# Kernel optimization log

Hardware: AMD Instinct MI355X
Metric: run time of the kernel (lower is better)

Reference implementation:

```python
import jax, jax.numpy as jnp
import numpy as np

B, S, D, F, E, K = 4, 2048, 1024, 2048, 8, 2


def setup_inputs() -> dict:
    key = jax.random.key(0)
    ks = jax.random.split(key, 6)
    s_in = 1.0 / np.sqrt(D)
    s_ff = 1.0 / np.sqrt(F)
    return {
        "x": jax.random.normal(ks[0], (B, S, D), jnp.float32),
        "rms_w": jnp.ones((D,), jnp.float32),
        "Wg": jax.random.normal(ks[1], (D, E), jnp.float32) * s_in,
        "bg": jnp.zeros((E,), jnp.float32),
        "W1a": jax.random.normal(ks[2], (E, D, F), jnp.float32) * s_in,
        "b1a": jnp.zeros((E, F), jnp.float32),
        "W1b": jax.random.normal(ks[3], (E, D, F), jnp.float32) * s_in,
        "b1b": jnp.zeros((E, F), jnp.float32),
        "W2": jax.random.normal(ks[4], (E, F, D), jnp.float32) * s_ff,
        "b2": jnp.zeros((E, D), jnp.float32),
    }


def reference(x, rms_w, Wg, bg, W1a, b1a, W1b, b1b, W2, b2):
    # RMSNorm (torch nn.RMSNorm with eps=None -> finfo eps)
    eps = jnp.finfo(x.dtype).eps
    x = x * jax.lax.rsqrt(jnp.mean(x * x, axis=-1, keepdims=True) + eps) * rms_w

    # top-k gating
    logits = x @ Wg + bg                              # [B,S,E]
    topk_vals, topk_idx = jax.lax.top_k(logits, K)    # [B,S,K]
    topk_w = jax.nn.softmax(topk_vals, axis=-1)       # [B,S,K]
    one_hot = jax.nn.one_hot(topk_idx, E, dtype=x.dtype)  # [B,S,K,E]
    weights = jnp.sum(one_hot * topk_w[..., None], axis=2)  # [B,S,E]

    # dense per-expert SwiGLU (faithful to the masked dense loop)
    a = jnp.einsum("bsd,edf->bsef", x, W1a) + b1a     # [B,S,E,F]
    b = jnp.einsum("bsd,edf->bsef", x, W1b) + b1b
    h = jax.nn.silu(a) * b
    y = jnp.einsum("bsef,efd->bsed", h, W2) + b2      # [B,S,E,D]
    out = jnp.einsum("bse,bsed->bsd", weights, y)     # [B,S,D]
    return out, weights
```

## Files before the change

### kernel.cpp

```cpp
#include <hip/hip_runtime.h>
#include <hip/hip_bf16.h>

#define DD 1024
#define FF 2048
#define EE 8
#define NT 8192
#define NRCAP 17280
#define MAXT128 135

typedef __attribute__((ext_vector_type(8))) short bf16x8;
typedef __attribute__((ext_vector_type(4))) float f32x4;

__device__ __forceinline__ ushort f2bf(float f) {
  __hip_bfloat16 h = __float2bfloat16(f);
  return *reinterpret_cast<ushort*>(&h);
}

__device__ __forceinline__ void gload16(const void* g, void* l) {
  __builtin_amdgcn_global_load_lds((const __attribute__((address_space(1))) void*)g,
                                   (__attribute__((address_space(3))) void*)l, 16, 0, 0);
}

__device__ __forceinline__ int swz_of_row(int r) { return ((r >> 1) & 3) << 4; }

__global__ __launch_bounds__(256) void k_transpose_all(
    const float* __restrict__ W1a, const float* __restrict__ W1b,
    const float* __restrict__ W2, ushort* __restrict__ BT1, ushort* __restrict__ W2T) {
  __shared__ ushort tile[64][68];
  const int z = blockIdx.z;
  const int cq = threadIdx.x & 15, rr = threadIdx.x >> 4;
  if (z < 16) {
    const int half = z >> 3, e = z & 7;
    const float* ip = (half ? W1b : W1a) + (size_t)e * DD * FF;
    const int f0 = blockIdx.x * 64, d0 = blockIdx.y * 64;
    #pragma unroll
    for (int p = 0; p < 4; p++) {
      const int r = rr + 16 * p;
      float4 v = *reinterpret_cast<const float4*>(ip + (size_t)(d0 + r) * FF + f0 + 4 * cq);
      *reinterpret_cast<ushort4*>(&tile[r][4 * cq]) =
          make_ushort4(f2bf(v.x), f2bf(v.y), f2bf(v.z), f2bf(v.w));
    }
    __syncthreads();
    ushort* op = BT1 + (size_t)e * 4096 * DD;
    const int rq = threadIdx.x & 15, cc = threadIdx.x >> 4;
    #pragma unroll
    for (int p = 0; p < 4; p++) {
      const int f = f0 + cc + 16 * p;
      const int rmap = ((f >> 4) << 5) + half * 16 + (f & 15);
      ushort4 u = make_ushort4(tile[4 * rq + 0][cc + 16 * p], tile[4 * rq + 1][cc + 16 * p],
                               tile[4 * rq + 2][cc + 16 * p], tile[4 * rq + 3][cc + 16 * p]);
      *reinterpret_cast<ushort4*>(op + (size_t)rmap * DD + d0 + 4 * rq) = u;
    }
  } else {
    const int e = z & 7;
    const float* ip = W2 + (size_t)e * FF * DD;
    const int r0 = blockIdx.x * 64;
    const int c0 = blockIdx.y * 64;
    #pragma unroll
    for (int p = 0; p < 4; p++) {
      const int r = rr + 16 * p;
      float4 v = *reinterpret_cast<const float4*>(ip + (size_t)(r0 + r) * DD + c0 + 4 * cq);
      *reinterpret_cast<ushort4*>(&tile[r][4 * cq]) =
          make_ushort4(f2bf(v.x), f2bf(v.y), f2bf(v.z), f2bf(v.w));
    }
    __syncthreads();
    ushort* op = W2T + (size_t)e * DD * FF;
    const int rq = threadIdx.x & 15, cc = threadIdx.x >> 4;
    #pragma unroll
    for (int p = 0; p < 4; p++) {
      const int c = cc + 16 * p;
      ushort4 u = make_ushort4(tile[4 * rq + 0][c], tile[4 * rq + 1][c],
                               tile[4 * rq + 2][c], tile[4 * rq + 3][c]);
      *reinterpret_cast<ushort4*>(op + (size_t)(c0 + c) * FF + r0 + 4 * rq) = u;
    }
  }
}

__global__ __launch_bounds__(256) void k_rms_gate(
    const float* __restrict__ x, const float* __restrict__ rms_w,
    const float* __restrict__ Wg, const float* __restrict__ bg,
    ushort* __restrict__ xn, float* __restrict__ out0, float* __restrict__ outW,
    int* __restrict__ tk_e, float* __restrict__ tk_w) {
  const int t = blockIdx.x * 4 + (threadIdx.x >> 6);
  const int lane = threadIdx.x & 63;
  const float* xrow = x + (size_t)t * DD;
  const float4* x4 = reinterpret_cast<const float4*>(xrow);
  const float4* w4 = reinterpret_cast<const float4*>(rms_w);
  const float4* Wg4 = reinterpret_cast<const float4*>(Wg);
  float4 xv[4];
  float ss = 0.f;
  #pragma unroll
  for (int i = 0; i < 4; i++) {
    xv[i] = x4[i * 64 + lane];
    ss += xv[i].x * xv[i].x + xv[i].y * xv[i].y + xv[i].z * xv[i].z + xv[i].w * xv[i].w;
  }
  #pragma unroll
  for (int m = 32; m; m >>= 1) ss += __shfl_xor(ss, m);
  const float sc = 1.0f / sqrtf(ss * (1.0f / (float)DD) + 1.1920929e-07f);
  ushort4* xout = reinterpret_cast<ushort4*>(xn + (size_t)t * DD);
  float4* orow = reinterpret_cast<float4*>(out0 + (size_t)t * DD);
  #pragma unroll
  for (int i = 0; i < 4; i++) {
    const float4 wv = w4[i * 64 + lane];
    xout[i * 64 + lane] = make_ushort4(f2bf(xv[i].x * sc * wv.x), f2bf(xv[i].y * sc * wv.y),
                                       f2bf(xv[i].z * sc * wv.z), f2bf(xv[i].w * sc * wv.w));
    orow[i * 64 + lane] = make_float4(0.f, 0.f, 0.f, 0.f);
  }
  float4 lgv = make_float4(0.f, 0.f, 0.f, 0.f);
  #pragma unroll 8
  for (int k = 0; k < 32; k++) {
    const int d = (lane >> 1) + 32 * k;
    const float s = xrow[d] * sc * rms_w[d];
    const float4 wg = Wg4[lane + 64 * k];
    lgv.x += s * wg.x; lgv.y += s * wg.y; lgv.z += s * wg.z; lgv.w += s * wg.w;
  }
  #pragma unroll
  for (int m = 32; m >= 2; m >>= 1) {
    lgv.x += __shfl_xor(lgv.x, m);
    lgv.y += __shfl_xor(lgv.y, m);
    lgv.z += __shfl_xor(lgv.z, m);
    lgv.w += __shfl_xor(lgv.w, m);
  }
  float4 other;
  other.x = __shfl(lgv.x, lane ^ 1);
  other.y = __shfl(lgv.y, lane ^ 1);
  other.z = __shfl(lgv.z, lane ^ 1);
  other.w = __shfl(lgv.w, lane ^ 1);
  if (lane == 0) {
    float l[8] = { lgv.x + bg[0], lgv.y + bg[1], lgv.z + bg[2], lgv.w + bg[3],
                   other.x + bg[4], other.y + bg[5], other.z + bg[6], other.w + bg[7] };
    int i0 = 0; float v0 = l[0];
    #pragma unroll
    for (int i = 1; i < 8; i++) if (l[i] > v0) { v0 = l[i]; i0 = i; }
    int i1 = -1; float v1 = -3.4e38f;
    #pragma unroll
    for (int i = 0; i < 8; i++) if (i != i0 && l[i] > v1) { v1 = l[i]; i1 = i; }
    const float e1v = __expf(v1 - v0);
    const float w0 = 1.0f / (1.0f + e1v);
    const float w1 = e1v * w0;
    float wout[8] = {0.f, 0.f, 0.f, 0.f, 0.f, 0.f, 0.f, 0.f};
    wout[i0] = w0; wout[i1] = w1;
    float4* wrow = reinterpret_cast<float4*>(outW + (size_t)t * EE);
    wrow[0] = make_float4(wout[0], wout[1], wout[2], wout[3]);
    wrow[1] = make_float4(wout[4], wout[5], wout[6], wout[7]);
    tk_e[t] = i0 | (i1 << 8);
    tk_w[2 * t] = w0; tk_w[2 * t + 1] = w1;
  }
}

__global__ __launch_bounds__(256) void k_scatter(
    const int* __restrict__ tk_e, const float* __restrict__ tk_w, int* __restrict__ base,
    int* __restrict__ tok_of_row, float* __restrict__ gw_of_row) {
  const int e = blockIdx.x;
  const int tid = threadIdx.x, wid = tid >> 6, lane = tid & 63;
  int c[8] = {0, 0, 0, 0, 0, 0, 0, 0};
  for (int i = tid; i < NT; i += 256) {
    const int ee = tk_e[i];
    c[ee & 255]++;
    c[(ee >> 8) & 255]++;
  }
  #pragma unroll
  for (int m = 32; m; m >>= 1) {
    #pragma unroll
    for (int i = 0; i < 8; i++) c[i] += __shfl_xor(c[i], m);
  }
  __shared__ int sw[4][8];
  __shared__ int s_base[9];
  if (lane == 0) {
    #pragma unroll
    for (int i = 0; i < 8; i++) sw[wid][i] = c[i];
  }
  __syncthreads();
  if (tid == 0) {
    int acc = 0;
    for (int q = 0; q < EE; q++) {
      s_base[q] = acc;
      const int cnt = sw[0][q] + sw[1][q] + sw[2][q] + sw[3][q];
      acc += ((cnt + 127) >> 7) << 7;
    }
    s_base[EE] = acc;
  }
  __syncthreads();
  if (e == 0 && tid <= EE) base[tid] = s_base[tid];
  const int myBase = s_base[e], myEnd = s_base[e + 1];
  for (int i = myBase + tid; i < myEnd; i += 256) tok_of_row[i] = -1;
  __syncthreads();
  __shared__ int s_cursor;
  __shared__ int s_woff[4];
  if (tid == 0) s_cursor = myBase;
  __syncthreads();
  for (int t0 = 0; t0 < NT; t0 += 256) {
    const int t = t0 + tid;
    const int ee = tk_e[t];
    const int m0 = (ee & 255) == e;
    const int m1 = ((ee >> 8) & 255) == e;
    const int has = m0 | m1;
    const unsigned long long mask = __ballot(has);
    const int prefix = __popcll(mask & ((1ull << lane) - 1ull));
    if (lane == 0) s_woff[wid] = __popcll(mask);
    __syncthreads();
    int woff = 0;
    #pragma unroll
    for (int w = 0; w < 4; w++) woff += (w < wid) ? s_woff[w] : 0;
    if (has) {
      const int row = s_cursor + woff + prefix;
      tok_of_row[row] = t;
      gw_of_row[row] = tk_w[2 * t + (m0 ? 0 : 1)];
    }
    __syncthreads();
    if (tid == 0) s_cursor += s_woff[0] + s_woff[1] + s_woff[2] + s_woff[3];
  }
}

__global__ __launch_bounds__(256) void k_ffn1(
    const ushort* __restrict__ xn, const ushort* __restrict__ BT1,
    const float* __restrict__ b1a, const float* __restrict__ b1b,
    const int* __restrict__ tok_of_row, const int* __restrict__ base,
    ushort* __restrict__ H) {
  const int row0 = blockIdx.y * 128;
  if (row0 >= base[EE]) return;
  int e = 0;
  while (e < EE - 1 && row0 >= base[e + 1]) e++;
  const int c0 = blockIdx.x * 128;
  const int tid = threadIdx.x, wid = tid >> 6, lane = tid & 63;
  const int wr = wid >> 1, wc = wid & 1;
  __shared__ __align__(16) ushort smem[128 * 72];
  ushort* sA = smem;
  ushort* sB = smem + 4096;
  const int rloc = tid >> 2;
  const int kcol = (((tid & 3) * 16) ^ swz_of_row(rloc)) >> 1;
  int tok0 = tok_of_row[row0 + rloc];      if (tok0 < 0) tok0 = 0;
  int tok1 = tok_of_row[row0 + 64 + rloc]; if (tok1 < 0) tok1 = 0;
  const ushort* gA0 = xn + (size_t)tok0 * DD + kcol;
  const ushort* gA1 = xn + (size_t)tok1 * DD + kcol;
  const ushort* gB0 = BT1 + ((size_t)e * 4096 + c0 + rloc) * DD + kcol;
  const ushort* gB1 = BT1 + ((size_t)e * 4096 + c0 + 64 + rloc) * DD + kcol;
  ushort* lA0 = sA + wid * 512;  ushort* lA1 = sA + 2048 + wid * 512;
  ushort* lB0 = sB + wid * 512;  ushort* lB1 = sB + 2048 + wid * 512;
  const int lrow = lane & 15, q = lane >> 4;
  const int fsw = (q * 16) ^ swz_of_row(lrow);
  int aoff[4], boff[4];
  #pragma unroll
  for (int m = 0; m < 4; m++) aoff[m] = (wr * 64 + m * 16 + lrow) * 64 + fsw;
  #pragma unroll
  for (int n = 0; n < 4; n++) boff[n] = (wc * 64 + n * 16 + lrow) * 64 + fsw;
  f32x4 acc[16];
  #pragma unroll
  for (int i = 0; i < 16; i++) acc[i] = (f32x4){0.f, 0.f, 0.f, 0.f};
  for (int kt = 0; kt < DD / 32; kt++) {
    gload16(gA0 + kt * 32, lA0);
    gload16(gA1 + kt * 32, lA1);
    gload16(gB0 + kt * 32, lB0);
    gload16(gB1 + kt * 32, lB1);
    __syncthreads();
    bf16x8 fb[4];
    #pragma unroll
    for (int n = 0; n < 4; n++)
      fb[n] = *reinterpret_cast<const bf16x8*>(reinterpret_cast<const char*>(sB) + boff[n]);
    #pragma unroll
    for (int m = 0; m < 4; m++) {
      const bf16x8 fa = *reinterpret_cast<const bf16x8*>(reinterpret_cast<const char*>(sA) + aoff[m]);
      #pragma unroll
      for (int n = 0; n < 4; n++)
        acc[m * 4 + n] = __builtin_amdgcn_mfma_f32_16x16x32_bf16(fa, fb[n], acc[m * 4 + n], 0, 0, 0);
    }
    __syncthreads();
  }
  #pragma unroll
  for (int np = 0; np < 2; np++) {
    const int fl = wc * 32 + np * 16 + lrow;
    const int f = (c0 >> 1) + fl;
    const float ba_ = b1a[e * FF + f], bb_ = b1b[e * FF + f];
    #pragma unroll
    for (int m = 0; m < 4; m++) {
      #pragma unroll
      for (int r = 0; r < 4; r++) {
        const float a = acc[m * 4 + 2 * np][r] + ba_;
        const float b = acc[m * 4 + 2 * np + 1][r] + bb_;
        const float h = (a / (1.0f + __expf(-a))) * b;
        const int rl = wr * 64 + m * 16 + q * 4 + r;
        smem[rl * 72 + fl] = f2bf(h);
      }
    }
  }
  __syncthreads();
  const int fc = tid & 7, rb = tid >> 3;
  #pragma unroll
  for (int i = 0; i < 4; i++) {
    const int rl = i * 32 + rb;
    const uint4 v = *reinterpret_cast<const uint4*>(&smem[rl * 72 + fc * 8]);
    *reinterpret_cast<uint4*>(H + (size_t)(row0 + rl) * FF + (c0 >> 1) + fc * 8) = v;
  }
}

__global__ __launch_bounds__(256) void k_ffn2(
    const ushort* __restrict__ H, const ushort* __restrict__ W2T, const float* __restrict__ b2,
    const int* __restrict__ tok_of_row, const float* __restrict__ gw_of_row,
    const int* __restrict__ base, float* __restrict__ out0) {
  const int row0 = blockIdx.y * 128;
  if (row0 >= base[EE]) return;
  int e = 0;
  while (e < EE - 1 && row0 >= base[e + 1]) e++;
  const int d0 = blockIdx.x * 128;
  const int tid = threadIdx.x, wid = tid >> 6, lane = tid & 63;
  const int wr = wid >> 1, wc = wid & 1;
  __shared__ ushort sA[128 * 32], sB[128 * 32];
  const int rloc = tid >> 2;
  const int kcol = (((tid & 3) * 16) ^ swz_of_row(rloc)) >> 1;
  const ushort* gA0 = H + (size_t)(row0 + rloc) * FF + kcol;
  const ushort* gA1 = H + (size_t)(row0 + 64 + rloc) * FF + kcol;
  const ushort* gB0 = W2T + ((size_t)e * DD + d0 + rloc) * FF + kcol;
  const ushort* gB1 = W2T + ((size_t)e * DD + d0 + 64 + rloc) * FF + kcol;
  ushort* lA0 = sA + wid * 512;  ushort* lA1 = sA + 2048 + wid * 512;
  ushort* lB0 = sB + wid * 512;  ushort* lB1 = sB + 2048 + wid * 512;
  const int lrow = lane & 15, q = lane >> 4;
  const int fsw = (q * 16) ^ swz_of_row(lrow);
  int aoff[4], boff[4];
  #pragma unroll
  for (int m = 0; m < 4; m++) aoff[m] = (wr * 64 + m * 16 + lrow) * 64 + fsw;
  #pragma unroll
  for (int n = 0; n < 4; n++) boff[n] = (wc * 64 + n * 16 + lrow) * 64 + fsw;
  f32x4 acc[16];
  #pragma unroll
  for (int i = 0; i < 16; i++) acc[i] = (f32x4){0.f, 0.f, 0.f, 0.f};
  for (int kt = 0; kt < FF / 32; kt++) {
    gload16(gA0 + kt * 32, lA0);
    gload16(gA1 + kt * 32, lA1);
    gload16(gB0 + kt * 32, lB0);
    gload16(gB1 + kt * 32, lB1);
    __syncthreads();
    bf16x8 fb[4];
    #pragma unroll
    for (int n = 0; n < 4; n++)
      fb[n] = *reinterpret_cast<const bf16x8*>(reinterpret_cast<const char*>(sB) + boff[n]);
    #pragma unroll
    for (int m = 0; m < 4; m++) {
      const bf16x8 fa = *reinterpret_cast<const bf16x8*>(reinterpret_cast<const char*>(sA) + aoff[m]);
      #pragma unroll
      for (int n = 0; n < 4; n++)
        acc[m * 4 + n] = __builtin_amdgcn_mfma_f32_16x16x32_bf16(fa, fb[n], acc[m * 4 + n], 0, 0, 0);
    }
    __syncthreads();
  }
  int dcols[4]; float bias[4];
  #pragma unroll
  for (int n = 0; n < 4; n++) {
    dcols[n] = d0 + wc * 64 + n * 16 + lrow;
    bias[n] = b2[e * DD + dcols[n]];
  }
  #pragma unroll
  for (int m = 0; m < 4; m++) {
    #pragma unroll
    for (int r = 0; r < 4; r++) {
      const int grow = row0 + wr * 64 + m * 16 + q * 4 + r;
      const int tk = tok_of_row[grow];
      if (tk >= 0) {
        const float gw = gw_of_row[grow];
        float* orow = out0 + (size_t)tk * DD;
        #pragma unroll
        for (int n = 0; n < 4; n++)
          atomicAdd(orow + dcols[n], gw * (acc[m * 4 + n][r] + bias[n]));
      }
    }
  }
}

#define WS_XN   ((size_t)0)
#define WS_BT1  ((size_t)16777216)
#define WS_W2T  ((size_t)83886080)
#define WS_H    ((size_t)117440512)
#define WS_TOK  ((size_t)188219392)
#define WS_GW   ((size_t)188288512)
#define WS_TKE  ((size_t)188357632)
#define WS_TKW  ((size_t)188390400)
#define WS_BASE ((size_t)188455936)

extern "C" void kernel_launch(void* const* d_in, const int* in_sizes, int n_in,
                              void* d_out, int out_size, void* d_ws, size_t ws_size,
                              hipStream_t stream) {
  const float* x     = (const float*)d_in[0];
  const float* rms_w = (const float*)d_in[1];
  const float* Wg    = (const float*)d_in[2];
  const float* bg    = (const float*)d_in[3];
  const float* W1a   = (const float*)d_in[4];
  const float* b1a   = (const float*)d_in[5];
  const float* W1b   = (const float*)d_in[6];
  const float* b1b   = (const float*)d_in[7];
  const float* W2    = (const float*)d_in[8];
  const float* b2    = (const float*)d_in[9];
  float* out0 = (float*)d_out;
  float* outW = (float*)d_out + (size_t)NT * DD;

  char* ws = (char*)d_ws;
  ushort* xn    = (ushort*)(ws + WS_XN);
  ushort* BT1   = (ushort*)(ws + WS_BT1);
  ushort* W2T   = (ushort*)(ws + WS_W2T);
  ushort* Hbuf  = (ushort*)(ws + WS_H);
  int*    tok   = (int*)(ws + WS_TOK);
  float*  gw    = (float*)(ws + WS_GW);
  int*    tk_e  = (int*)(ws + WS_TKE);
  float*  tk_w  = (float*)(ws + WS_TKW);
  int*    base  = (int*)(ws + WS_BASE);

  k_transpose_all<<<dim3(32, 16, 24), 256, 0, stream>>>(W1a, W1b, W2, BT1, W2T);

  k_rms_gate<<<NT / 4, 256, 0, stream>>>(x, rms_w, Wg, bg, xn, out0, outW, tk_e, tk_w);
  k_scatter<<<EE, 256, 0, stream>>>(tk_e, tk_w, base, tok, gw);

  k_ffn1<<<dim3(4096 / 128, MAXT128), 256, 0, stream>>>(xn, BT1, b1a, b1b, tok, base, Hbuf);
  k_ffn2<<<dim3(DD / 128, MAXT128), 256, 0, stream>>>(Hbuf, W2T, b2, tok, gw, base, out0);
}
```

Before: 436.0 us.

## Replace atomic scatter-add in FFN2 with dense Y buffer plus per-token gather

FFN2 now writes its per-row expert outputs plus bias into a dense fp32 Y buffer instead of doing gate-weighted atomicAdds into the output. A new gather kernel then combines each token's two rows with its top-k weights. The scatter kernel records the Y row for each token slot instead of a per-row gate weight, and the output zero-init in rms_gate is dropped. This removes atomic contention and the zeroing pass. In exchange it costs a roughly 70MB intermediate write and read, one extra launch, and a Y buffer that aliases the xn/BT1 workspace.

```diff
diff --git a/kernel.cpp b/kernel.cpp
--- a/kernel.cpp
+++ b/kernel.cpp
@@ -79,7 +79,7 @@
 __global__ __launch_bounds__(256) void k_rms_gate(
     const float* __restrict__ x, const float* __restrict__ rms_w,
     const float* __restrict__ Wg, const float* __restrict__ bg,
-    ushort* __restrict__ xn, float* __restrict__ out0, float* __restrict__ outW,
+    ushort* __restrict__ xn, float* __restrict__ outW,
     int* __restrict__ tk_e, float* __restrict__ tk_w) {
   const int t = blockIdx.x * 4 + (threadIdx.x >> 6);
   const int lane = threadIdx.x & 63;
@@ -98,13 +98,11 @@
   for (int m = 32; m; m >>= 1) ss += __shfl_xor(ss, m);
   const float sc = 1.0f / sqrtf(ss * (1.0f / (float)DD) + 1.1920929e-07f);
   ushort4* xout = reinterpret_cast<ushort4*>(xn + (size_t)t * DD);
-  float4* orow = reinterpret_cast<float4*>(out0 + (size_t)t * DD);
   #pragma unroll
   for (int i = 0; i < 4; i++) {
     const float4 wv = w4[i * 64 + lane];
     xout[i * 64 + lane] = make_ushort4(f2bf(xv[i].x * sc * wv.x), f2bf(xv[i].y * sc * wv.y),
                                        f2bf(xv[i].z * sc * wv.z), f2bf(xv[i].w * sc * wv.w));
-    orow[i * 64 + lane] = make_float4(0.f, 0.f, 0.f, 0.f);
   }
   float4 lgv = make_float4(0.f, 0.f, 0.f, 0.f);
   #pragma unroll 8
@@ -149,8 +147,8 @@
 }
 
 __global__ __launch_bounds__(256) void k_scatter(
-    const int* __restrict__ tk_e, const float* __restrict__ tk_w, int* __restrict__ base,
-    int* __restrict__ tok_of_row, float* __restrict__ gw_of_row) {
+    const int* __restrict__ tk_e, int* __restrict__ base,
+    int* __restrict__ tok_of_row, int* __restrict__ rows_of_tok) {
   const int e = blockIdx.x;
   const int tid = threadIdx.x, wid = tid >> 6, lane = tid & 63;
   int c[8] = {0, 0, 0, 0, 0, 0, 0, 0};
@@ -205,7 +203,7 @@
     if (has) {
       const int row = s_cursor + woff + prefix;
       tok_of_row[row] = t;
-      gw_of_row[row] = tk_w[2 * t + (m0 ? 0 : 1)];
+      rows_of_tok[2 * t + (m0 ? 0 : 1)] = row;
     }
     __syncthreads();
     if (tid == 0) s_cursor += s_woff[0] + s_woff[1] + s_woff[2] + s_woff[3];
@@ -295,8 +293,7 @@
 
 __global__ __launch_bounds__(256) void k_ffn2(
     const ushort* __restrict__ H, const ushort* __restrict__ W2T, const float* __restrict__ b2,
-    const int* __restrict__ tok_of_row, const float* __restrict__ gw_of_row,
-    const int* __restrict__ base, float* __restrict__ out0) {
+    const int* __restrict__ base, float* __restrict__ Y) {
   const int row0 = blockIdx.y * 128;
   if (row0 >= base[EE]) return;
   int e = 0;
@@ -342,38 +339,48 @@
     }
     __syncthreads();
   }
-  int dcols[4]; float bias[4];
   #pragma unroll
   for (int n = 0; n < 4; n++) {
-    dcols[n] = d0 + wc * 64 + n * 16 + lrow;
-    bias[n] = b2[e * DD + dcols[n]];
-  }
-  #pragma unroll
-  for (int m = 0; m < 4; m++) {
-    #pragma unroll
-    for (int r = 0; r < 4; r++) {
-      const int grow = row0 + wr * 64 + m * 16 + q * 4 + r;
-      const int tk = tok_of_row[grow];
-      if (tk >= 0) {
-        const float gw = gw_of_row[grow];
-        float* orow = out0 + (size_t)tk * DD;
-        #pragma unroll
-        for (int n = 0; n < 4; n++)
-          atomicAdd(orow + dcols[n], gw * (acc[m * 4 + n][r] + bias[n]));
+    const int dcol = d0 + wc * 64 + n * 16 + lrow;
+    const float bias = b2[e * DD + dcol];
+    #pragma unroll
+    for (int m = 0; m < 4; m++) {
+      #pragma unroll
+      for (int r = 0; r < 4; r++) {
+        const int grow = row0 + wr * 64 + m * 16 + q * 4 + r;
+        Y[(size_t)grow * DD + dcol] = acc[m * 4 + n][r] + bias;
       }
     }
   }
 }
 
+__global__ __launch_bounds__(256) void k_gather(
+    const float* __restrict__ Y, const int* __restrict__ rows_of_tok,
+    const float* __restrict__ tk_w, float* __restrict__ out0) {
+  for (int t = blockIdx.x; t < NT; t += gridDim.x) {
+    const int r0 = rows_of_tok[2 * t], r1 = rows_of_tok[2 * t + 1];
+    const float w0 = tk_w[2 * t], w1 = tk_w[2 * t + 1];
+    const float4 y0 = reinterpret_cast<const float4*>(Y + (size_t)r0 * DD)[threadIdx.x];
+    const float4 y1 = reinterpret_cast<const float4*>(Y + (size_t)r1 * DD)[threadIdx.x];
+    float4 o;
+    o.x = w0 * y0.x + w1 * y1.x;
+    o.y = w0 * y0.y + w1 * y1.y;
+    o.z = w0 * y0.z + w1 * y1.z;
+    o.w = w0 * y0.w + w1 * y1.w;
+    reinterpret_cast<float4*>(out0 + (size_t)t * DD)[threadIdx.x] = o;
+  }
+}
+
+#define WS_Y    ((size_t)0)
 #define WS_XN   ((size_t)0)
 #define WS_BT1  ((size_t)16777216)
 #define WS_W2T  ((size_t)83886080)
 #define WS_H    ((size_t)117440512)
 #define WS_TOK  ((size_t)188219392)
-#define WS_GW   ((size_t)188288512)
-#define WS_TKE  ((size_t)188357632)
-#define WS_TKW  ((size_t)188390400)
-#define WS_BASE ((size_t)188455936)
+#define WS_ROWS ((size_t)188288512)
+#define WS_TKE  ((size_t)188354048)
+#define WS_TKW  ((size_t)188386816)
+#define WS_BASE ((size_t)188452352)
 
 extern "C" void kernel_launch(void* const* d_in, const int* in_sizes, int n_in,
                               void* d_out, int out_size, void* d_ws, size_t ws_size,
@@ -396,17 +403,19 @@
   ushort* BT1   = (ushort*)(ws + WS_BT1);
   ushort* W2T   = (ushort*)(ws + WS_W2T);
   ushort* Hbuf  = (ushort*)(ws + WS_H);
+  float*  Ybuf  = (float*)(ws + WS_Y);
   int*    tok   = (int*)(ws + WS_TOK);
-  float*  gw    = (float*)(ws + WS_GW);
+  int*    rows  = (int*)(ws + WS_ROWS);
   int*    tk_e  = (int*)(ws + WS_TKE);
   float*  tk_w  = (float*)(ws + WS_TKW);
   int*    base  = (int*)(ws + WS_BASE);
 
   k_transpose_all<<<dim3(32, 16, 24), 256, 0, stream>>>(W1a, W1b, W2, BT1, W2T);
 
-  k_rms_gate<<<NT / 4, 256, 0, stream>>>(x, rms_w, Wg, bg, xn, out0, outW, tk_e, tk_w);
-  k_scatter<<<EE, 256, 0, stream>>>(tk_e, tk_w, base, tok, gw);
+  k_rms_gate<<<NT / 4, 256, 0, stream>>>(x, rms_w, Wg, bg, xn, outW, tk_e, tk_w);
+  k_scatter<<<EE, 256, 0, stream>>>(tk_e, base, tok, rows);
 
   k_ffn1<<<dim3(4096 / 128, MAXT128), 256, 0, stream>>>(xn, BT1, b1a, b1b, tok, base, Hbuf);
-  k_ffn2<<<dim3(DD / 128, MAXT128), 256, 0, stream>>>(Hbuf, W2T, b2, tok, gw, base, out0);
-}
+  k_ffn2<<<dim3(DD / 128, MAXT128), 256, 0, stream>>>(Hbuf, W2T, b2, base, Ybuf);
+  k_gather<<<2048, 256, 0, stream>>>(Ybuf, rows, tk_w, out0);
+}
```

Measured after the change: 398.5 us, median of 2. 8.6% less time.

## Replace output atomics with per-slot stores plus a sum kernel; fuse front kernels

Applied to the files above, without the earlier changes.

Merges the weight-transpose and RMSNorm/gating kernels into one launch, using block-index ranges to pick the role. The second FFN now stores each token's gated expert output into one of two slot buffers (chosen by top-k rank) instead of doing float atomicAdds into the output. A new elementwise kernel then sums the two slots into the output. This removes atomic contention and the output zeroing, at the cost of an extra 64 MB scratch write and a read-add-write pass. The slot buffer is placed over the xn/BT1 workspace, which is only safe because those buffers are consumed before the second FFN runs.

```diff
diff --git a/kernel.cpp b/kernel.cpp
--- a/kernel.cpp
+++ b/kernel.cpp
@@ -23,16 +23,89 @@
 
 __device__ __forceinline__ int swz_of_row(int r) { return ((r >> 1) & 3) << 4; }
 
-__global__ __launch_bounds__(256) void k_transpose_all(
-    const float* __restrict__ W1a, const float* __restrict__ W1b,
-    const float* __restrict__ W2, ushort* __restrict__ BT1, ushort* __restrict__ W2T) {
+__global__ __launch_bounds__(256) void k_front(
+    const float* __restrict__ x, const float* __restrict__ rms_w,
+    const float* __restrict__ Wg, const float* __restrict__ bg,
+    const float* __restrict__ W1a, const float* __restrict__ W1b, const float* __restrict__ W2,
+    ushort* __restrict__ xn, float* __restrict__ outW,
+    int* __restrict__ tk_e, float* __restrict__ tk_w,
+    ushort* __restrict__ BT1, ushort* __restrict__ W2T) {
   __shared__ ushort tile[64][68];
-  const int z = blockIdx.z;
+  const int bid = blockIdx.x;
+  if (bid < 2048) {
+    const int t = bid * 4 + (threadIdx.x >> 6);
+    const int lane = threadIdx.x & 63;
+    const float* xrow = x + (size_t)t * DD;
+    const float4* x4 = reinterpret_cast<const float4*>(xrow);
+    const float4* w4 = reinterpret_cast<const float4*>(rms_w);
+    const float4* Wg4 = reinterpret_cast<const float4*>(Wg);
+    float4 xv[4];
+    float ss = 0.f;
+    #pragma unroll
+    for (int i = 0; i < 4; i++) {
+      xv[i] = x4[i * 64 + lane];
+      ss += xv[i].x * xv[i].x + xv[i].y * xv[i].y + xv[i].z * xv[i].z + xv[i].w * xv[i].w;
+    }
+    #pragma unroll
+    for (int m = 32; m; m >>= 1) ss += __shfl_xor(ss, m);
+    const float sc = 1.0f / sqrtf(ss * (1.0f / (float)DD) + 1.1920929e-07f);
+    ushort4* xout = reinterpret_cast<ushort4*>(xn + (size_t)t * DD);
+    #pragma unroll
+    for (int i = 0; i < 4; i++) {
+      const float4 wv = w4[i * 64 + lane];
+      xout[i * 64 + lane] = make_ushort4(f2bf(xv[i].x * sc * wv.x), f2bf(xv[i].y * sc * wv.y),
+                                         f2bf(xv[i].z * sc * wv.z), f2bf(xv[i].w * sc * wv.w));
+    }
+    float4 lgv = make_float4(0.f, 0.f, 0.f, 0.f);
+    #pragma unroll 8
+    for (int k = 0; k < 32; k++) {
+      const int d = (lane >> 1) + 32 * k;
+      const float s = xrow[d] * sc * rms_w[d];
+      const float4 wg = Wg4[lane + 64 * k];
+      lgv.x += s * wg.x; lgv.y += s * wg.y; lgv.z += s * wg.z; lgv.w += s * wg.w;
+    }
+    #pragma unroll
+    for (int m = 32; m >= 2; m >>= 1) {
+      lgv.x += __shfl_xor(lgv.x, m);
+      lgv.y += __shfl_xor(lgv.y, m);
+      lgv.z += __shfl_xor(lgv.z, m);
+      lgv.w += __shfl_xor(lgv.w, m);
+    }
+    float4 other;
+    other.x = __shfl(lgv.x, lane ^ 1);
+    other.y = __shfl(lgv.y, lane ^ 1);
+    other.z = __shfl(lgv.z, lane ^ 1);
+    other.w = __shfl(lgv.w, lane ^ 1);
+    if (lane == 0) {
+      float l[8] = { lgv.x + bg[0], lgv.y + bg[1], lgv.z + bg[2], lgv.w + bg[3],
+                     other.x + bg[4], other.y + bg[5], other.z + bg[6], other.w + bg[7] };
+      int i0 = 0; float v0 = l[0];
+      #pragma unroll
+      for (int i = 1; i < 8; i++) if (l[i] > v0) { v0 = l[i]; i0 = i; }
+      int i1 = -1; float v1 = -3.4e38f;
+      #pragma unroll
+      for (int i = 0; i < 8; i++) if (i != i0 && l[i] > v1) { v1 = l[i]; i1 = i; }
+      const float e1v = __expf(v1 - v0);
+      const float w0 = 1.0f / (1.0f + e1v);
+      const float w1 = e1v * w0;
+      float wout[8] = {0.f, 0.f, 0.f, 0.f, 0.f, 0.f, 0.f, 0.f};
+      wout[i0] = w0; wout[i1] = w1;
+      float4* wrow = reinterpret_cast<float4*>(outW + (size_t)t * EE);
+      wrow[0] = make_float4(wout[0], wout[1], wout[2], wout[3]);
+      wrow[1] = make_float4(wout[4], wout[5], wout[6], wout[7]);
+      tk_e[t] = i0 | (i1 << 8);
+      tk_w[2 * t] = w0; tk_w[2 * t + 1] = w1;
+    }
+    return;
+  }
+  const int tb = bid - 2048;
+  const int z = tb >> 9, rem = tb & 511;
+  const int bx = rem & 31, by = rem >> 5;
   const int cq = threadIdx.x & 15, rr = threadIdx.x >> 4;
   if (z < 16) {
     const int half = z >> 3, e = z & 7;
     const float* ip = (half ? W1b : W1a) + (size_t)e * DD * FF;
-    const int f0 = blockIdx.x * 64, d0 = blockIdx.y * 64;
+    const int f0 = bx * 64, d0 = by * 64;
     #pragma unroll
     for (int p = 0; p < 4; p++) {
       const int r = rr + 16 * p;
@@ -54,8 +127,8 @@
   } else {
     const int e = z & 7;
     const float* ip = W2 + (size_t)e * FF * DD;
-    const int r0 = blockIdx.x * 64;
-    const int c0 = blockIdx.y * 64;
+    const int r0 = bx * 64;
+    const int c0 = by * 64;
     #pragma unroll
     for (int p = 0; p < 4; p++) {
       const int r = rr + 16 * p;
@@ -76,81 +149,9 @@
   }
 }
 
-__global__ __launch_bounds__(256) void k_rms_gate(
-    const float* __restrict__ x, const float* __restrict__ rms_w,
-    const float* __restrict__ Wg, const float* __restrict__ bg,
-    ushort* __restrict__ xn, float* __restrict__ out0, float* __restrict__ outW,
-    int* __restrict__ tk_e, float* __restrict__ tk_w) {
-  const int t = blockIdx.x * 4 + (threadIdx.x >> 6);
-  const int lane = threadIdx.x & 63;
-  const float* xrow = x + (size_t)t * DD;
-  const float4* x4 = reinterpret_cast<const float4*>(xrow);
-  const float4* w4 = reinterpret_cast<const float4*>(rms_w);
-  const float4* Wg4 = reinterpret_cast<const float4*>(Wg);
-  float4 xv[4];
-  float ss = 0.f;
-  #pragma unroll
-  for (int i = 0; i < 4; i++) {
-    xv[i] = x4[i * 64 + lane];
-    ss += xv[i].x * xv[i].x + xv[i].y * xv[i].y + xv[i].z * xv[i].z + xv[i].w * xv[i].w;
-  }
-  #pragma unroll
-  for (int m = 32; m; m >>= 1) ss += __shfl_xor(ss, m);
-  const float sc = 1.0f / sqrtf(ss * (1.0f / (float)DD) + 1.1920929e-07f);
-  ushort4* xout = reinterpret_cast<ushort4*>(xn + (size_t)t * DD);
-  float4* orow = reinterpret_cast<float4*>(out0 + (size_t)t * DD);
-  #pragma unroll
-  for (int i = 0; i < 4; i++) {
-    const float4 wv = w4[i * 64 + lane];
-    xout[i * 64 + lane] = make_ushort4(f2bf(xv[i].x * sc * wv.x), f2bf(xv[i].y * sc * wv.y),
-                                       f2bf(xv[i].z * sc * wv.z), f2bf(xv[i].w * sc * wv.w));
-    orow[i * 64 + lane] = make_float4(0.f, 0.f, 0.f, 0.f);
-  }
-  float4 lgv = make_float4(0.f, 0.f, 0.f, 0.f);
-  #pragma unroll 8
-  for (int k = 0; k < 32; k++) {
-    const int d = (lane >> 1) + 32 * k;
-    const float s = xrow[d] * sc * rms_w[d];
-    const float4 wg = Wg4[lane + 64 * k];
-    lgv.x += s * wg.x; lgv.y += s * wg.y; lgv.z += s * wg.z; lgv.w += s * wg.w;
-  }
-  #pragma unroll
-  for (int m = 32; m >= 2; m >>= 1) {
-    lgv.x += __shfl_xor(lgv.x, m);
-    lgv.y += __shfl_xor(lgv.y, m);
-    lgv.z += __shfl_xor(lgv.z, m);
-    lgv.w += __shfl_xor(lgv.w, m);
-  }
-  float4 other;
-  other.x = __shfl(lgv.x, lane ^ 1);
-  other.y = __shfl(lgv.y, lane ^ 1);
-  other.z = __shfl(lgv.z, lane ^ 1);
-  other.w = __shfl(lgv.w, lane ^ 1);
-  if (lane == 0) {
-    float l[8] = { lgv.x + bg[0], lgv.y + bg[1], lgv.z + bg[2], lgv.w + bg[3],
-                   other.x + bg[4], other.y + bg[5], other.z + bg[6], other.w + bg[7] };
-    int i0 = 0; float v0 = l[0];
-    #pragma unroll
-    for (int i = 1; i < 8; i++) if (l[i] > v0) { v0 = l[i]; i0 = i; }
-    int i1 = -1; float v1 = -3.4e38f;
-    #pragma unroll
-    for (int i = 0; i < 8; i++) if (i != i0 && l[i] > v1) { v1 = l[i]; i1 = i; }
-    const float e1v = __expf(v1 - v0);
-    const float w0 = 1.0f / (1.0f + e1v);
-    const float w1 = e1v * w0;
-    float wout[8] = {0.f, 0.f, 0.f, 0.f, 0.f, 0.f, 0.f, 0.f};
-    wout[i0] = w0; wout[i1] = w1;
-    float4* wrow = reinterpret_cast<float4*>(outW + (size_t)t * EE);
-    wrow[0] = make_float4(wout[0], wout[1], wout[2], wout[3]);
-    wrow[1] = make_float4(wout[4], wout[5], wout[6], wout[7]);
-    tk_e[t] = i0 | (i1 << 8);
-    tk_w[2 * t] = w0; tk_w[2 * t + 1] = w1;
-  }
-}
-
 __global__ __launch_bounds__(256) void k_scatter(
     const int* __restrict__ tk_e, const float* __restrict__ tk_w, int* __restrict__ base,
-    int* __restrict__ tok_of_row, float* __restrict__ gw_of_row) {
+    int* __restrict__ tok_of_row, int* __restrict__ dst_of_row, float* __restrict__ gw_of_row) {
   const int e = blockIdx.x;
   const int tid = threadIdx.x, wid = tid >> 6, lane = tid & 63;
   int c[8] = {0, 0, 0, 0, 0, 0, 0, 0};
@@ -183,7 +184,10 @@
   __syncthreads();
   if (e == 0 && tid <= EE) base[tid] = s_base[tid];
   const int myBase = s_base[e], myEnd = s_base[e + 1];
-  for (int i = myBase + tid; i < myEnd; i += 256) tok_of_row[i] = -1;
+  for (int i = myBase + tid; i < myEnd; i += 256) {
+    tok_of_row[i] = -1;
+    dst_of_row[i] = -1;
+  }
   __syncthreads();
   __shared__ int s_cursor;
   __shared__ int s_woff[4];
@@ -204,8 +208,10 @@
     for (int w = 0; w < 4; w++) woff += (w < wid) ? s_woff[w] : 0;
     if (has) {
       const int row = s_cursor + woff + prefix;
+      const int slot = m0 ? 0 : 1;
       tok_of_row[row] = t;
-      gw_of_row[row] = tk_w[2 * t + (m0 ? 0 : 1)];
+      dst_of_row[row] = slot * NT + t;
+      gw_of_row[row] = tk_w[2 * t + slot];
     }
     __syncthreads();
     if (tid == 0) s_cursor += s_woff[0] + s_woff[1] + s_woff[2] + s_woff[3];
@@ -295,8 +301,8 @@
 
 __global__ __launch_bounds__(256) void k_ffn2(
     const ushort* __restrict__ H, const ushort* __restrict__ W2T, const float* __restrict__ b2,
-    const int* __restrict__ tok_of_row, const float* __restrict__ gw_of_row,
-    const int* __restrict__ base, float* __restrict__ out0) {
+    const int* __restrict__ dst_of_row, const float* __restrict__ gw_of_row,
+    const int* __restrict__ base, float* __restrict__ Yslot) {
   const int row0 = blockIdx.y * 128;
   if (row0 >= base[EE]) return;
   int e = 0;
@@ -353,27 +359,41 @@
     #pragma unroll
     for (int r = 0; r < 4; r++) {
       const int grow = row0 + wr * 64 + m * 16 + q * 4 + r;
-      const int tk = tok_of_row[grow];
-      if (tk >= 0) {
+      const int dst = dst_of_row[grow];
+      if (dst >= 0) {
         const float gw = gw_of_row[grow];
-        float* orow = out0 + (size_t)tk * DD;
+        float* orow = Yslot + (size_t)dst * DD;
         #pragma unroll
         for (int n = 0; n < 4; n++)
-          atomicAdd(orow + dcols[n], gw * (acc[m * 4 + n][r] + bias[n]));
+          orow[dcols[n]] = gw * (acc[m * 4 + n][r] + bias[n]);
       }
     }
   }
 }
 
+__global__ __launch_bounds__(256) void k_add(
+    const float* __restrict__ Yslot, float* __restrict__ out0) {
+  const float4* y0 = reinterpret_cast<const float4*>(Yslot);
+  const float4* y1 = reinterpret_cast<const float4*>(Yslot + (size_t)NT * DD);
+  float4* o = reinterpret_cast<float4*>(out0);
+  const int n4 = NT * DD / 4;
+  for (int i = blockIdx.x * 256 + threadIdx.x; i < n4; i += gridDim.x * 256) {
+    const float4 a = y0[i], b = y1[i];
+    o[i] = make_float4(a.x + b.x, a.y + b.y, a.z + b.z, a.w + b.w);
+  }
+}
+
+#define WS_YS   ((size_t)0)
 #define WS_XN   ((size_t)0)
 #define WS_BT1  ((size_t)16777216)
 #define WS_W2T  ((size_t)83886080)
 #define WS_H    ((size_t)117440512)
 #define WS_TOK  ((size_t)188219392)
-#define WS_GW   ((size_t)188288512)
-#define WS_TKE  ((size_t)188357632)
-#define WS_TKW  ((size_t)188390400)
-#define WS_BASE ((size_t)188455936)
+#define WS_DST  ((size_t)188288512)
+#define WS_GW   ((size_t)188357632)
+#define WS_TKE  ((size_t)188426752)
+#define WS_TKW  ((size_t)188459520)
+#define WS_BASE ((size_t)188525056)
 
 extern "C" void kernel_launch(void* const* d_in, const int* in_sizes, int n_in,
                               void* d_out, int out_size, void* d_ws, size_t ws_size,
@@ -396,17 +416,19 @@
   ushort* BT1   = (ushort*)(ws + WS_BT1);
   ushort* W2T   = (ushort*)(ws + WS_W2T);
   ushort* Hbuf  = (ushort*)(ws + WS_H);
+  float*  Yslot = (float*)(ws + WS_YS);
   int*    tok   = (int*)(ws + WS_TOK);
+  int*    dst   = (int*)(ws + WS_DST);
   float*  gw    = (float*)(ws + WS_GW);
   int*    tk_e  = (int*)(ws + WS_TKE);
   float*  tk_w  = (float*)(ws + WS_TKW);
   int*    base  = (int*)(ws + WS_BASE);
 
-  k_transpose_all<<<dim3(32, 16, 24), 256, 0, stream>>>(W1a, W1b, W2, BT1, W2T);
-
-  k_rms_gate<<<NT / 4, 256, 0, stream>>>(x, rms_w, Wg, bg, xn, out0, outW, tk_e, tk_w);
-  k_scatter<<<EE, 256, 0, stream>>>(tk_e, tk_w, base, tok, gw);
+  k_front<<<14336, 256, 0, stream>>>(x, rms_w, Wg, bg, W1a, W1b, W2,
+                                     xn, outW, tk_e, tk_w, BT1, W2T);
+  k_scatter<<<EE, 256, 0, stream>>>(tk_e, tk_w, base, tok, dst, gw);
 
   k_ffn1<<<dim3(4096 / 128, MAXT128), 256, 0, stream>>>(xn, BT1, b1a, b1b, tok, base, Hbuf);
-  k_ffn2<<<dim3(DD / 128, MAXT128), 256, 0, stream>>>(Hbuf, W2T, b2, tok, gw, base, out0);
-}
+  k_ffn2<<<dim3(DD / 128, MAXT128), 256, 0, stream>>>(Hbuf, W2T, b2, dst, gw, base, Yslot);
+  k_add<<<2048, 256, 0, stream>>>(Yslot, out0);
+}
```

Result: faster. 411.0 us (-5.8%).
